# Optimization experiments

Hardware: AMD Instinct MI355X
Metric: run time of the kernel (lower is better)

Reference implementation:

```python
import jax, jax.numpy as jnp
import numpy as np

T = 5       # fixed temporal factor in the original forward
HEADS = 8
DIM = 512
DIM_HEAD = 64
INNER = HEADS * DIM_HEAD  # 512 (must equal DIM for the masked scatter)


def setup_inputs() -> dict:
    key = jax.random.key(0)
    ks = jax.random.split(key, 8)
    bt, n = 40, 3137  # b=8, t=5; n-1 = 56*56 visual tokens
    x = jax.random.normal(ks[0], (bt, n, DIM), dtype=jnp.float32)
    mask = jax.random.randint(ks[1], (bt, 56, 56), 0, 2).astype(jnp.float32)
    s = 1.0 / np.sqrt(DIM)
    w_vq = jax.random.normal(ks[2], (DIM, INNER), dtype=jnp.float32) * s
    w_vkv = jax.random.normal(ks[3], (DIM, 2 * INNER), dtype=jnp.float32) * s
    w_aqkv = jax.random.normal(ks[4], (DIM, 3 * INNER), dtype=jnp.float32) * s
    w_out = jax.random.normal(ks[5], (INNER, DIM), dtype=jnp.float32) * s
    b_out = jnp.zeros((DIM,), dtype=jnp.float32)
    return {"x": x, "mask": mask, "w_vq": w_vq, "w_vkv": w_vkv,
            "w_aqkv": w_aqkv, "w_out": w_out, "b_out": b_out}


def reference(x, mask, w_vq, w_vkv, w_aqkv, w_out, b_out):
    bt, n, dim = x.shape
    b = bt // T
    nv = n - 1
    dh = DIM_HEAD
    scale = dh ** -0.5

    A = x[:, 0]        # (bt, dim) -- single 'action' token per frame
    V = x[:, 1:]       # (bt, nv, dim)
    m = mask.reshape(bt, nv, 1)

    aq, ak, av = jnp.split(A @ w_aqkv, 3, axis=-1)      # each (bt, INNER)
    vk, vv = jnp.split(V @ w_vkv, 2, axis=-1)           # each (bt, nv, INNER)
    vq = V @ w_vq                                        # (bt, nv, INNER)

    # --- A -> V cross attention: per batch, T A-queries over T*nv V keys ---
    qa = aq.reshape(b, T, HEADS, dh)
    Kv = vk.reshape(b, T * nv, HEADS, dh)
    Vv = vv.reshape(b, T * nv, HEADS, dh)
    av_dots = jnp.einsum('bqhd,bkhd->bhqk', qa, Kv) * scale
    av_attn = jax.nn.softmax(av_dots, axis=-1)
    av_o = jnp.einsum('bhqk,bkhd->bqhd', av_attn, Vv)   # (b, T, H, dh)
    a_out = av_o.reshape(bt, 1, INNER)

    # --- V -> A cross attention with block mask: every V token attends only
    # to its own batch's T A-tokens (the -inf block fill in the original) ---
    Qv = vq.reshape(b, T, nv, HEADS, dh)
    Ka = ak.reshape(b, T, HEADS, dh)
    Va = av.reshape(b, T, HEADS, dh)
    va_dots = jnp.einsum('bfnhd,bkhd->bhfnk', Qv, Ka) * scale
    va_attn = jax.nn.softmax(va_dots, axis=-1)          # softmax over T keys
    va_o = jnp.einsum('bhfnk,bkhd->bfnhd', va_attn, Va)
    v_full = va_o.reshape(bt, nv, INNER)

    # original: scatter attn out into V.clone() then * mask, under no_grad()
    # => masked positions get attention output, others V*0 = 0; detached.
    v_out = jax.lax.stop_gradient(v_full * m)

    out = jnp.concatenate([a_out, v_out], axis=1)       # (bt, n, INNER)
    return out @ w_out + b_out
```

## Files before the change

### kernel.cpp

```cpp
#include <hip/hip_runtime.h>

typedef unsigned short u16;
typedef unsigned int u32;
typedef __attribute__((ext_vector_type(8))) u16 u16x8;
typedef __attribute__((ext_vector_type(8))) __bf16 bf16x8;
typedef __attribute__((ext_vector_type(4))) float f32x4;

__device__ __forceinline__ float b2f(u16 u){ return __uint_as_float(((u32)u)<<16); }
__device__ __forceinline__ u16 f2b(float f){
  u32 b = __float_as_uint(f);
  return (u16)((b + 0x7fffu + ((b>>16)&1u))>>16);
}
__device__ __forceinline__ void gload16(const void* g, void* l){
  __builtin_amdgcn_global_load_lds((__attribute__((address_space(1))) void*)g,
                                   (__attribute__((address_space(3))) void*)l, 16, 0, 0);
}
__device__ __forceinline__ float wred_max(float v){
#pragma unroll
  for (int o=32;o>0;o>>=1) v = fmaxf(v, __shfl_xor(v,o));
  return v;
}
__device__ __forceinline__ float wred_sum(float v){
#pragma unroll
  for (int o=32;o>0;o>>=1) v += __shfl_xor(v,o);
  return v;
}

__global__ void k_cast_x(const float* __restrict__ x, u16* __restrict__ xb, int n8){
  int stride = gridDim.x*blockDim.x;
  for (int i = blockIdx.x*blockDim.x + threadIdx.x; i < n8; i += stride){
    const float4* p = (const float4*)(x + (size_t)i*8);
    float4 a = p[0], b = p[1];
    u16x8 o;
    o[0]=f2b(a.x); o[1]=f2b(a.y); o[2]=f2b(a.z); o[3]=f2b(a.w);
    o[4]=f2b(b.x); o[5]=f2b(b.y); o[6]=f2b(b.z); o[7]=f2b(b.w);
    *(u16x8*)(xb + (size_t)i*8) = o;
  }
}

__global__ void k_prep_w(const float* __restrict__ wvq, const float* __restrict__ wvkv,
                         const float* __restrict__ wout, u16* __restrict__ W1T,
                         u16* __restrict__ WoutT){
  int id = blockIdx.x*blockDim.x + threadIdx.x;
  if (id < 786432){
    int n = id >> 9, k = id & 511;
    float v = (n < 512) ? wvq[k*512 + n] : wvkv[k*1024 + (n-512)];
    W1T[id] = f2b(v);
  } else {
    int j = id - 786432;
    int n = j >> 9, k = j & 511;
    WoutT[j] = f2b(wout[k*512 + n]);
  }
}

__global__ void k_agent_qkv(const float* __restrict__ x, const float* __restrict__ w,
                            float* __restrict__ aqkv){
  int id = blockIdx.x*blockDim.x + threadIdx.x;
  int bt = id / 1536, c = id % 1536;
  const float* xr = x + (size_t)bt*3137*512;
  float s = 0.f;
  for (int k=0;k<512;k++) s += xr[k]*w[k*1536+c];
  aqkv[id] = s;
}

template<int FOUT>
__global__ __launch_bounds__(256) void k_gemm_bt(
    const u16* __restrict__ A, const u16* __restrict__ BT,
    int M, int N, int K, int NX,
    u16* __restrict__ Cb, float* __restrict__ Cf, const float* __restrict__ bias)
{
  __shared__ __align__(16) char Asm[128*64*2];
  __shared__ __align__(16) char Bsm[128*64*2];
  const int tid = threadIdx.x;
  const int wid = tid >> 6, lane = tid & 63;
  const int nwg = gridDim.x;
  const int orig = blockIdx.x;
  const int q8 = nwg >> 3, r8 = nwg & 7;
  const int xc = orig & 7, sl = orig >> 3;
  const int work = (xc < r8 ? xc*(q8+1) : r8*(q8+1) + (xc-r8)*q8) + sl;
  const int m0 = (work / NX) * 128, n0 = (work % NX) * 128;
  const char* Ab = (const char*)A;
  const char* Bb = (const char*)BT;
  size_t aoff[4], boff[4];
  int ldsoff[4];
#pragma unroll
  for (int i=0;i<4;i++){
    int L = i*4096 + wid*1024 + lane*16;
    int r = L >> 7;
    int cb = (L ^ ((r&7)<<4)) & 127;
    ldsoff[i] = i*4096 + wid*1024;
    int ra = m0 + r; if (ra >= M) ra = M-1;
    aoff[i] = (size_t)ra*(size_t)(K*2) + cb;
    boff[i] = (size_t)(n0 + r)*(size_t)(K*2) + cb;
  }
  f32x4 acc[4][4] = {};
  const int wm = (wid>>1)*64, wn = (wid&1)*64;

  for (int k0 = 0; k0 < K; k0 += 64){
#pragma unroll
    for (int i=0;i<4;i++){
      gload16(Ab + aoff[i] + k0*2, Asm + ldsoff[i]);
      gload16(Bb + boff[i] + k0*2, Bsm + ldsoff[i]);
    }
    __syncthreads();
#pragma unroll
    for (int kk=0;kk<2;kk++){
      const int cb = kk*64 + ((lane>>4)<<4);
      bf16x8 af[4], bfr[4];
#pragma unroll
      for (int mr=0;mr<4;mr++){
        int r = wm + mr*16 + (lane&15);
        af[mr] = *(const bf16x8*)(Asm + r*128 + (cb ^ ((r&7)<<4)));
      }
#pragma unroll
      for (int nc=0;nc<4;nc++){
        int r = wn + nc*16 + (lane&15);
        bfr[nc] = *(const bf16x8*)(Bsm + r*128 + (cb ^ ((r&7)<<4)));
      }
#pragma unroll
      for (int mr=0;mr<4;mr++)
#pragma unroll
        for (int nc=0;nc<4;nc++)
          acc[mr][nc] = __builtin_amdgcn_mfma_f32_16x16x32_bf16(af[mr], bfr[nc], acc[mr][nc], 0,0,0);
    }
    __syncthreads();
  }
  if (m0 + 128 <= M){
#pragma unroll
    for (int mr=0;mr<4;mr++){
#pragma unroll
      for (int nc=0;nc<4;nc++){
#pragma unroll
        for (int rg=0;rg<4;rg++){
          int row = m0 + wm + mr*16 + ((lane>>4)<<2) + rg;
          int col = n0 + wn + nc*16 + (lane&15);
          float v = acc[mr][nc][rg];
          if (FOUT) Cf[(size_t)row*N + col] = v + bias[col];
          else      Cb[(size_t)row*N + col] = f2b(v);
        }
      }
    }
  } else {
#pragma unroll
    for (int mr=0;mr<4;mr++){
#pragma unroll
      for (int nc=0;nc<4;nc++){
#pragma unroll
        for (int rg=0;rg<4;rg++){
          int row = m0 + wm + mr*16 + ((lane>>4)<<2) + rg;
          int col = n0 + wn + nc*16 + (lane&15);
          if (row < M){
            float v = acc[mr][nc][rg];
            if (FOUT) Cf[(size_t)row*N + col] = v + bias[col];
            else      Cb[(size_t)row*N + col] = f2b(v);
          }
        }
      }
    }
  }
}

__global__ __launch_bounds__(320) void k_attn_agent(
    const u16* __restrict__ out1, const float* __restrict__ aqkv,
    float* __restrict__ pm, float* __restrict__ pl, float* __restrict__ pacc)
{
  __shared__ __align__(16) char Ksm[16384];
  __shared__ __align__(16) char Vsm[16384];
  const int bid = blockIdx.x;
  const int sp = bid & 15, bh = bid >> 4, b = bh >> 3, h = bh & 7;
  const int tid = threadIdx.x, wid = tid >> 6, lane = tid & 63;
  const int q = wid;
  float qreg[64];
  {
    const float* ap = aqkv + ((size_t)(b*5+q)*1536 + h*64);
#pragma unroll
    for (int d=0; d<64; d++) qreg[d] = ap[d];
  }
  float m = -1e30f, l = 0.f;
  float acc[8] = {0,0,0,0,0,0,0,0};
  const int g0 = sp * 980;
  for (int c = 0; c < 8; c++){
    for (int idx = tid; idx < 2048; idx += 320){
      int arr = idx >> 10, rem = idx & 1023;
      int r = rem >> 3, seg = rem & 7;
      int loc = c*128 + r; if (loc > 979) loc = 979;
      int gk = g0 + loc;
      int tk = gk / 3136, nv = gk - tk*3136;
      size_t grow = (size_t)((b*5+tk)*3137 + 1 + nv)*1536 + (arr ? 1024 : 512) + h*64 + seg*8;
      u16x8 v = *(const u16x8*)(out1 + grow);
      char* dst = arr ? Vsm : Ksm;
      *(u16x8*)(dst + r*128 + ((seg*16) ^ ((r&7)<<4))) = v;
    }
    __syncthreads();
    float s0 = 0.f, s1 = 0.f;
#pragma unroll
    for (int seg=0; seg<8; seg++){
      const int r0 = lane, r1 = 64 + lane;
      u16x8 k0 = *(const u16x8*)(Ksm + r0*128 + ((seg*16) ^ ((r0&7)<<4)));
      u16x8 k1 = *(const u16x8*)(Ksm + r1*128 + ((seg*16) ^ ((r1&7)<<4)));
#pragma unroll
      for (int j=0;j<8;j++){
        s0 += qreg[seg*8+j]*b2f(k0[j]);
        s1 += qreg[seg*8+j]*b2f(k1[j]);
      }
    }
    s0 *= 0.125f; s1 *= 0.125f;
    const int locbase = c*128;
    if (locbase + lane >= 980)      s0 = -1e30f;
    if (locbase + 64 + lane >= 980) s1 = -1e30f;
    float cmax = wred_max(fmaxf(s0, s1));
    float mn = fmaxf(m, cmax);
    float resc = __expf(m - mn);
    float p0 = (s0 > -1e29f) ? __expf(s0 - mn) : 0.f;
    float p1 = (s1 > -1e29f) ? __expf(s1 - mn) : 0.f;
    l = l*resc + wred_sum(p0 + p1);
#pragma unroll
    for (int j=0;j<8;j++) acc[j] *= resc;
    const int g = lane >> 3, cc = lane & 7;
#pragma unroll
    for (int i=0;i<16;i++){
      int k = i*8 + g;
      u16x8 vv = *(const u16x8*)(Vsm + k*128 + ((cc*16) ^ ((k&7)<<4)));
      float p = (i < 8) ? __shfl(p0, k) : __shfl(p1, k-64);
#pragma unroll
      for (int j=0;j<8;j++) acc[j] += p*b2f(vv[j]);
    }
    m = mn;
    __syncthreads();
  }
#pragma unroll
  for (int j=0;j<8;j++){
    float v = acc[j];
    v += __shfl_xor(v, 8); v += __shfl_xor(v, 16); v += __shfl_xor(v, 32);
    acc[j] = v;
  }
  const int base = (bh*16 + sp)*5 + q;
  if (lane == 0){ pm[base] = m; pl[base] = l; }
  if (lane < 8){
    float* pa = pacc + (size_t)base*64 + lane*8;
#pragma unroll
    for (int j=0;j<8;j++) pa[j] = acc[j];
  }
}

__global__ void k_agent_combine(const float* __restrict__ pm, const float* __restrict__ pl,
                                const float* __restrict__ pacc, u16* __restrict__ IN)
{
  const int id = blockIdx.x;
  const int q = id % 5, t2 = id / 5;
  const int h = t2 & 7, b = t2 >> 3;
  const int d = threadIdx.x;
  const int bh = b*8 + h;
  float ms = -1e30f;
#pragma unroll
  for (int s2=0;s2<16;s2++) ms = fmaxf(ms, pm[(bh*16+s2)*5+q]);
  float L = 0.f, o = 0.f;
#pragma unroll
  for (int s2=0;s2<16;s2++){
    int base = (bh*16+s2)*5+q;
    float w = __expf(pm[base]-ms);
    L += w*pl[base];
    o += w*pacc[(size_t)base*64 + d];
  }
  IN[(size_t)(b*5+q)*3137*512 + h*64 + d] = f2b(o / L);
}

__global__ __launch_bounds__(256) void k_attn_frame(
    const u16* __restrict__ out1, const float* __restrict__ aqkv,
    const float* __restrict__ mask, u16* __restrict__ IN)
{
  __shared__ float Ka[5][8][68];
  __shared__ float Va[5][8][68];
  const int b = blockIdx.y;
  const int tid = threadIdx.x;
  for (int i = tid; i < 2560; i += 256){
    int t = i >> 9, rem = i & 511, hh = rem >> 6, d = rem & 63;
    const float* src = aqkv + (size_t)(b*5+t)*1536;
    Ka[t][hh][d] = src[512 + hh*64 + d];
    Va[t][hh][d] = src[1024 + hh*64 + d];
  }
  __syncthreads();
  const int task = blockIdx.x*256 + tid;
  const int h = task & 7, rl = task >> 3;
  const int f = rl / 3136, nv = rl - f*3136;
  const int bt = b*5 + f;
  const size_t r1 = (size_t)bt*3137 + 1 + nv;
  const u16* qp = out1 + r1*1536 + h*64;
  float qf[64];
#pragma unroll
  for (int sg=0; sg<8; sg++){
    u16x8 v = *(const u16x8*)(qp + sg*8);
#pragma unroll
    for (int j=0;j<8;j++) qf[sg*8+j] = b2f(v[j]);
  }
  float sd[5];
#pragma unroll
  for (int t=0;t<5;t++){
    float s = 0.f;
#pragma unroll
    for (int d=0;d<64;d++) s += qf[d]*Ka[t][h][d];
    sd[t] = s*0.125f;
  }
  float mx = sd[0];
#pragma unroll
  for (int t=1;t<5;t++) mx = fmaxf(mx, sd[t]);
  float p[5], ps = 0.f;
#pragma unroll
  for (int t=0;t<5;t++){ p[t] = __expf(sd[t]-mx); ps += p[t]; }
  const float mv = mask[(size_t)bt*3136 + nv] / ps;
  u16* op = IN + r1*512 + h*64;
#pragma unroll
  for (int sg=0; sg<8; sg++){
    u16x8 o;
#pragma unroll
    for (int j=0;j<8;j++){
      const int d = sg*8+j;
      float v = 0.f;
#pragma unroll
      for (int t=0;t<5;t++) v += p[t]*Va[t][h][d];
      o[j] = f2b(v*mv);
    }
    *(u16x8*)(op + sg*8) = o;
  }
}

extern "C" void kernel_launch(void* const* d_in, const int* in_sizes, int n_in,
                              void* d_out, int out_size, void* d_ws, size_t ws_size,
                              hipStream_t stream)
{
  const float* x      = (const float*)d_in[0];
  const float* mask   = (const float*)d_in[1];
  const float* w_vq   = (const float*)d_in[2];
  const float* w_vkv  = (const float*)d_in[3];
  const float* w_aqkv = (const float*)d_in[4];
  const float* w_out  = (const float*)d_in[5];
  const float* b_out  = (const float*)d_in[6];
  float* out = (float*)d_out;
  char* ws = (char*)d_ws;

  constexpr size_t MR = 125480;
  constexpr size_t OFF_XB   = 0;
  constexpr size_t OFF_OUT1 = OFF_XB + MR*512*2;
  constexpr size_t OFF_W1T  = OFF_OUT1 + MR*1536*2;
  constexpr size_t OFF_WOT  = OFF_W1T + 1536*512*2;
  constexpr size_t OFF_AQKV = OFF_WOT + 512*512*2;
  constexpr size_t OFF_PM   = OFF_W1T;
  constexpr size_t OFF_PL   = OFF_PM + 5120*4;
  constexpr size_t OFF_PACC = OFF_PL + 5120*4;

  u16* Xb     = (u16*)(ws + OFF_XB);
  u16* out1   = (u16*)(ws + OFF_OUT1);
  u16* W1T    = (u16*)(ws + OFF_W1T);
  u16* WoutT  = (u16*)(ws + OFF_WOT);
  float* aqkv = (float*)(ws + OFF_AQKV);
  float* pm   = (float*)(ws + OFF_PM);
  float* pl   = (float*)(ws + OFF_PL);
  float* pacc = (float*)(ws + OFF_PACC);

  k_cast_x<<<2048, 256, 0, stream>>>(x, Xb, 8030720);
  k_prep_w<<<4096, 256, 0, stream>>>(w_vq, w_vkv, w_out, W1T, WoutT);
  k_agent_qkv<<<240, 256, 0, stream>>>(x, w_aqkv, aqkv);
  k_gemm_bt<0><<<11772, 256, 0, stream>>>(Xb, W1T, (int)MR, 1536, 512, 12, out1, nullptr, nullptr);
  k_attn_agent<<<1024, 320, 0, stream>>>(out1, aqkv, pm, pl, pacc);
  k_attn_frame<<<dim3(490,8), 256, 0, stream>>>(out1, aqkv, mask, Xb);
  k_agent_combine<<<320, 64, 0, stream>>>(pm, pl, pacc, Xb);
  k_gemm_bt<1><<<3924, 256, 0, stream>>>(Xb, WoutT, (int)MR, 512, 512, 4, nullptr, out, b_out);
}
```

Measured before the change: 860.9 us.

## Fuse per-frame V->A attention into QKV GEMM epilogue and merge prep kernels

The GEMM epilogue for the Vq column tiles now computes the 5-key softmax attention against the agent K/V directly from the accumulators. It writes masked outputs straight into the IN buffer, so the Vq half of out1 is never stored to or reloaded from global memory and the separate frame-attention kernel is removed. The three preprocessing kernels (x cast, weight transpose, agent QKV) are merged into one launch. The price is a heavier epilogue with cross-lane shuffles, and a dependency on each 128-row tile spanning at most two batches.

Measured after the change: 905.8 us. +5.2%, slower.

```diff
diff --git a/kernel.cpp b/kernel.cpp
--- a/kernel.cpp
+++ b/kernel.cpp
@@ -26,55 +26,56 @@
   return v;
 }
 
-__global__ void k_cast_x(const float* __restrict__ x, u16* __restrict__ xb, int n8){
-  int stride = gridDim.x*blockDim.x;
-  for (int i = blockIdx.x*blockDim.x + threadIdx.x; i < n8; i += stride){
-    const float4* p = (const float4*)(x + (size_t)i*8);
-    float4 a = p[0], b = p[1];
-    u16x8 o;
-    o[0]=f2b(a.x); o[1]=f2b(a.y); o[2]=f2b(a.z); o[3]=f2b(a.w);
-    o[4]=f2b(b.x); o[5]=f2b(b.y); o[6]=f2b(b.z); o[7]=f2b(b.w);
-    *(u16x8*)(xb + (size_t)i*8) = o;
-  }
-}
-
-__global__ void k_prep_w(const float* __restrict__ wvq, const float* __restrict__ wvkv,
-                         const float* __restrict__ wout, u16* __restrict__ W1T,
-                         u16* __restrict__ WoutT){
-  int id = blockIdx.x*blockDim.x + threadIdx.x;
-  if (id < 786432){
-    int n = id >> 9, k = id & 511;
-    float v = (n < 512) ? wvq[k*512 + n] : wvkv[k*1024 + (n-512)];
-    W1T[id] = f2b(v);
+__global__ void k_pre(const float* __restrict__ x, const float* __restrict__ wvq,
+                      const float* __restrict__ wvkv, const float* __restrict__ wout,
+                      const float* __restrict__ waqkv,
+                      u16* __restrict__ xb, u16* __restrict__ W1T,
+                      u16* __restrict__ WoutT, float* __restrict__ aqkv){
+  const int bid = blockIdx.x, tid = threadIdx.x;
+  if (bid < 2048){
+    const int stride = 2048*256;
+    for (int i = bid*256 + tid; i < 8030720; i += stride){
+      const float4* p = (const float4*)(x + (size_t)i*8);
+      float4 a = p[0], b = p[1];
+      u16x8 o;
+      o[0]=f2b(a.x); o[1]=f2b(a.y); o[2]=f2b(a.z); o[3]=f2b(a.w);
+      o[4]=f2b(b.x); o[5]=f2b(b.y); o[6]=f2b(b.z); o[7]=f2b(b.w);
+      *(u16x8*)(xb + (size_t)i*8) = o;
+    }
+  } else if (bid < 6144){
+    int id = (bid-2048)*256 + tid;
+    if (id < 786432){
+      int n = id >> 9, k = id & 511;
+      float v = (n < 512) ? wvq[k*512 + n] : wvkv[k*1024 + (n-512)];
+      W1T[id] = f2b(v);
+    } else {
+      int j = id - 786432;
+      int n = j >> 9, k = j & 511;
+      WoutT[j] = f2b(wout[k*512 + n]);
+    }
   } else {
-    int j = id - 786432;
-    int n = j >> 9, k = j & 511;
-    WoutT[j] = f2b(wout[k*512 + n]);
-  }
-}
-
-__global__ void k_agent_qkv(const float* __restrict__ x, const float* __restrict__ w,
-                            float* __restrict__ aqkv){
-  int id = blockIdx.x*blockDim.x + threadIdx.x;
-  int bt = id / 1536, c = id % 1536;
-  const float* xr = x + (size_t)bt*3137*512;
-  float s = 0.f;
-  for (int k=0;k<512;k++) s += xr[k]*w[k*1536+c];
-  aqkv[id] = s;
+    int id = (bid-6144)*256 + tid;
+    int bt = id / 1536, c = id % 1536;
+    const float* xr = x + (size_t)bt*3137*512;
+    float s = 0.f;
+    for (int k=0;k<512;k++) s += xr[k]*waqkv[k*1536+c];
+    aqkv[id] = s;
+  }
 }
 
 template<int FOUT>
 __global__ __launch_bounds__(256) void k_gemm_bt(
     const u16* __restrict__ A, const u16* __restrict__ BT,
     int M, int N, int K, int NX,
-    u16* __restrict__ Cb, float* __restrict__ Cf, const float* __restrict__ bias)
+    u16* __restrict__ Cb, float* __restrict__ Cf, const float* __restrict__ bias,
+    u16* __restrict__ IN, const float* __restrict__ aqkv,
+    const float* __restrict__ mask)
 {
   __shared__ __align__(16) char Asm[128*64*2];
   __shared__ __align__(16) char Bsm[128*64*2];
   const int tid = threadIdx.x;
   const int wid = tid >> 6, lane = tid & 63;
-  const int nwg = gridDim.x;
-  const int orig = blockIdx.x;
+  const int nwg = gridDim.x, orig = blockIdx.x;
   const int q8 = nwg >> 3, r8 = nwg & 7;
   const int xc = orig & 7, sl = orig >> 3;
   const int work = (xc < r8 ? xc*(q8+1) : r8*(q8+1) + (xc-r8)*q8) + sl;
@@ -125,34 +126,95 @@
     }
     __syncthreads();
   }
-  if (m0 + 128 <= M){
+
+  if (FOUT == 0 && n0 < 512){
+    float* akL = (float*)Asm;
+    float* avL = (float*)(Asm + 5120);
+    const int b0 = m0 / 15685;
+    const int h0 = n0 >> 6;
+    for (int i = tid; i < 1280; i += 256){
+      int bi = i / 640, rem = i - bi*640;
+      int t = rem >> 7, rem2 = rem & 127;
+      int hh = rem2 >> 6, d = rem2 & 63;
+      int bsel = b0 + bi; if (bsel > 7) bsel = 7;
+      const float* src = aqkv + (size_t)(bsel*5 + t)*1536 + (h0+hh)*64 + d;
+      akL[i] = src[512];
+      avL[i] = src[1024];
+    }
+    __syncthreads();
+    const int ln = lane & 15, lq = lane >> 4;
+    const int hh = wid & 1;
+    const int thr1 = (b0+1)*15685;
 #pragma unroll
     for (int mr=0;mr<4;mr++){
 #pragma unroll
-      for (int nc=0;nc<4;nc++){
-#pragma unroll
-        for (int rg=0;rg<4;rg++){
-          int row = m0 + wm + mr*16 + ((lane>>4)<<2) + rg;
-          int col = n0 + wn + nc*16 + (lane&15);
-          float v = acc[mr][nc][rg];
-          if (FOUT) Cf[(size_t)row*N + col] = v + bias[col];
-          else      Cb[(size_t)row*N + col] = f2b(v);
+      for (int rg=0;rg<4;rg++){
+        const int row = m0 + wm + mr*16 + lq*4 + rg;
+        const int bi = (row >= thr1) ? 1 : 0;
+        float pt[5];
+#pragma unroll
+        for (int t=0;t<5;t++){
+          const float* ak = akL + ((bi*5+t)*2 + hh)*64 + ln;
+          pt[t] = acc[mr][0][rg]*ak[0]  + acc[mr][1][rg]*ak[16]
+                + acc[mr][2][rg]*ak[32] + acc[mr][3][rg]*ak[48];
+        }
+#pragma unroll
+        for (int off=1; off<16; off<<=1){
+#pragma unroll
+          for (int t=0;t<5;t++) pt[t] += __shfl_xor(pt[t], off);
+        }
+        float mx = fmaxf(fmaxf(fmaxf(pt[0],pt[1]),fmaxf(pt[2],pt[3])),pt[4]);
+        float ps = 0.f;
+#pragma unroll
+        for (int t=0;t<5;t++){ pt[t] = __expf((pt[t]-mx)*0.125f); ps += pt[t]; }
+        const int bt = row / 3137;
+        const int j  = row - bt*3137;
+        const float mvv = (j > 0 && row < M) ? mask[(size_t)bt*3136 + (j-1)] : 0.f;
+        const float mv = mvv / ps;
+        if (row < M){
+          u16* op = IN + (size_t)row*512 + (h0+hh)*64 + ln;
+#pragma unroll
+          for (int nc=0;nc<4;nc++){
+            const float* av = avL + ((bi*5)*2 + hh)*64 + nc*16 + ln;
+            float o = pt[0]*av[0] + pt[1]*av[128] + pt[2]*av[256]
+                    + pt[3]*av[384] + pt[4]*av[512];
+            op[nc*16] = f2b(o*mv);
+          }
         }
       }
     }
   } else {
-#pragma unroll
-    for (int mr=0;mr<4;mr++){
-#pragma unroll
-      for (int nc=0;nc<4;nc++){
-#pragma unroll
-        for (int rg=0;rg<4;rg++){
-          int row = m0 + wm + mr*16 + ((lane>>4)<<2) + rg;
-          int col = n0 + wn + nc*16 + (lane&15);
-          if (row < M){
+    const int cshift = (FOUT == 0) ? 512 : 0;
+    const int NW = (FOUT == 0) ? 1024 : N;
+    if (m0 + 128 <= M){
+#pragma unroll
+      for (int mr=0;mr<4;mr++){
+#pragma unroll
+        for (int nc=0;nc<4;nc++){
+#pragma unroll
+          for (int rg=0;rg<4;rg++){
+            int row = m0 + wm + mr*16 + ((lane>>4)<<2) + rg;
+            int col = n0 + wn + nc*16 + (lane&15) - cshift;
             float v = acc[mr][nc][rg];
-            if (FOUT) Cf[(size_t)row*N + col] = v + bias[col];
-            else      Cb[(size_t)row*N + col] = f2b(v);
+            if (FOUT) Cf[(size_t)row*NW + col] = v + bias[col];
+            else      Cb[(size_t)row*NW + col] = f2b(v);
+          }
+        }
+      }
+    } else {
+#pragma unroll
+      for (int mr=0;mr<4;mr++){
+#pragma unroll
+        for (int nc=0;nc<4;nc++){
+#pragma unroll
+          for (int rg=0;rg<4;rg++){
+            int row = m0 + wm + mr*16 + ((lane>>4)<<2) + rg;
+            int col = n0 + wn + nc*16 + (lane&15) - cshift;
+            if (row < M){
+              float v = acc[mr][nc][rg];
+              if (FOUT) Cf[(size_t)row*NW + col] = v + bias[col];
+              else      Cb[(size_t)row*NW + col] = f2b(v);
+            }
           }
         }
       }
@@ -186,7 +248,7 @@
       int loc = c*128 + r; if (loc > 979) loc = 979;
       int gk = g0 + loc;
       int tk = gk / 3136, nv = gk - tk*3136;
-      size_t grow = (size_t)((b*5+tk)*3137 + 1 + nv)*1536 + (arr ? 1024 : 512) + h*64 + seg*8;
+      size_t grow = (size_t)((b*5+tk)*3137 + 1 + nv)*1024 + (arr ? 512 : 0) + h*64 + seg*8;
       u16x8 v = *(const u16x8*)(out1 + grow);
       char* dst = arr ? Vsm : Ksm;
       *(u16x8*)(dst + r*128 + ((seg*16) ^ ((r&7)<<4))) = v;
@@ -243,8 +305,8 @@
   }
 }
 
-__global__ void k_agent_combine(const float* __restrict__ pm, const float* __restrict__ pl,
-                                const float* __restrict__ pacc, u16* __restrict__ IN)
+__global__ void k_combine(const float* __restrict__ pm, const float* __restrict__ pl,
+                          const float* __restrict__ pacc, u16* __restrict__ IN)
 {
   const int id = blockIdx.x;
   const int q = id % 5, t2 = id / 5;
@@ -263,65 +325,6 @@
     o += w*pacc[(size_t)base*64 + d];
   }
   IN[(size_t)(b*5+q)*3137*512 + h*64 + d] = f2b(o / L);
-}
-
-__global__ __launch_bounds__(256) void k_attn_frame(
-    const u16* __restrict__ out1, const float* __restrict__ aqkv,
-    const float* __restrict__ mask, u16* __restrict__ IN)
-{
-  __shared__ float Ka[5][8][68];
-  __shared__ float Va[5][8][68];
-  const int b = blockIdx.y;
-  const int tid = threadIdx.x;
-  for (int i = tid; i < 2560; i += 256){
-    int t = i >> 9, rem = i & 511, hh = rem >> 6, d = rem & 63;
-    const float* src = aqkv + (size_t)(b*5+t)*1536;
-    Ka[t][hh][d] = src[512 + hh*64 + d];
-    Va[t][hh][d] = src[1024 + hh*64 + d];
-  }
-  __syncthreads();
-  const int task = blockIdx.x*256 + tid;
-  const int h = task & 7, rl = task >> 3;
-  const int f = rl / 3136, nv = rl - f*3136;
-  const int bt = b*5 + f;
-  const size_t r1 = (size_t)bt*3137 + 1 + nv;
-  const u16* qp = out1 + r1*1536 + h*64;
-  float qf[64];
-#pragma unroll
-  for (int sg=0; sg<8; sg++){
-    u16x8 v = *(const u16x8*)(qp + sg*8);
-#pragma unroll
-    for (int j=0;j<8;j++) qf[sg*8+j] = b2f(v[j]);
-  }
-  float sd[5];
-#pragma unroll
-  for (int t=0;t<5;t++){
-    float s = 0.f;
-#pragma unroll
-    for (int d=0;d<64;d++) s += qf[d]*Ka[t][h][d];
-    sd[t] = s*0.125f;
-  }
-  float mx = sd[0];
-#pragma unroll
-  for (int t=1;t<5;t++) mx = fmaxf(mx, sd[t]);
-  float p[5], ps = 0.f;
-#pragma unroll
-  for (int t=0;t<5;t++){ p[t] = __expf(sd[t]-mx); ps += p[t]; }
-  const float mv = mask[(size_t)bt*3136 + nv] / ps;
-  u16* op = IN + r1*512 + h*64;
-#pragma unroll
-  for (int sg=0; sg<8; sg++){
-    u16x8 o;
-#pragma unroll
-    for (int j=0;j<8;j++){
-      const int d = sg*8+j;
-      float v = 0.f;
-#pragma unroll
-      for (int t=0;t<5;t++) v += p[t]*Va[t][h][d];
-      o[j] = f2b(v*mv);
-    }
-    *(u16x8*)(op + sg*8) = o;
-  }
 }
 
 extern "C" void kernel_launch(void* const* d_in, const int* in_sizes, int n_in,
@@ -340,16 +343,18 @@
 
   constexpr size_t MR = 125480;
   constexpr size_t OFF_XB   = 0;
-  constexpr size_t OFF_OUT1 = OFF_XB + MR*512*2;
-  constexpr size_t OFF_W1T  = OFF_OUT1 + MR*1536*2;
+  constexpr size_t OFF_KV   = OFF_XB + MR*512*2;
+  constexpr size_t OFF_IN   = OFF_KV + MR*1024*2;
+  constexpr size_t OFF_W1T  = OFF_IN + MR*512*2;
   constexpr size_t OFF_WOT  = OFF_W1T + 1536*512*2;
   constexpr size_t OFF_AQKV = OFF_WOT + 512*512*2;
-  constexpr size_t OFF_PM   = OFF_W1T;
+  constexpr size_t OFF_PM   = OFF_AQKV + 40*1536*4;
   constexpr size_t OFF_PL   = OFF_PM + 5120*4;
   constexpr size_t OFF_PACC = OFF_PL + 5120*4;
 
   u16* Xb     = (u16*)(ws + OFF_XB);
-  u16* out1   = (u16*)(ws + OFF_OUT1);
+  u16* out1kv = (u16*)(ws + OFF_KV);
+  u16* IN     = (u16*)(ws + OFF_IN);
   u16* W1T    = (u16*)(ws + OFF_W1T);
   u16* WoutT  = (u16*)(ws + OFF_WOT);
   float* aqkv = (float*)(ws + OFF_AQKV);
@@ -357,12 +362,11 @@
   float* pl   = (float*)(ws + OFF_PL);
   float* pacc = (float*)(ws + OFF_PACC);
 
-  k_cast_x<<<2048, 256, 0, stream>>>(x, Xb, 8030720);
-  k_prep_w<<<4096, 256, 0, stream>>>(w_vq, w_vkv, w_out, W1T, WoutT);
-  k_agent_qkv<<<240, 256, 0, stream>>>(x, w_aqkv, aqkv);
-  k_gemm_bt<0><<<11772, 256, 0, stream>>>(Xb, W1T, (int)MR, 1536, 512, 12, out1, nullptr, nullptr);
-  k_attn_agent<<<1024, 320, 0, stream>>>(out1, aqkv, pm, pl, pacc);
-  k_attn_frame<<<dim3(490,8), 256, 0, stream>>>(out1, aqkv, mask, Xb);
-  k_agent_combine<<<320, 64, 0, stream>>>(pm, pl, pacc, Xb);
-  k_gemm_bt<1><<<3924, 256, 0, stream>>>(Xb, WoutT, (int)MR, 512, 512, 4, nullptr, out, b_out);
-}
+  k_pre<<<6384, 256, 0, stream>>>(x, w_vq, w_vkv, w_out, w_aqkv, Xb, W1T, WoutT, aqkv);
+  k_gemm_bt<0><<<11772, 256, 0, stream>>>(Xb, W1T, (int)MR, 1536, 512, 12,
+                                          out1kv, nullptr, nullptr, IN, aqkv, mask);
+  k_attn_agent<<<1024, 320, 0, stream>>>(out1kv, aqkv, pm, pl, pacc);
+  k_combine<<<320, 64, 0, stream>>>(pm, pl, pacc, IN);
+  k_gemm_bt<1><<<3924, 256, 0, stream>>>(IN, WoutT, (int)MR, 512, 512, 4,
+                                         nullptr, out, b_out, nullptr, nullptr, nullptr);
+}
```
